# Kernel tuning notes

Measured on AMD Instinct MI355X. Metric: run time of the kernel, lower is better.

## Reference

```python
import jax, jax.numpy as jnp
import numpy as np

N = 8192      # nodes (64 graphs x 128 nodes)
E = 131072    # edges (avg degree 16)
G = 64        # graphs
F_IN = 64     # num_node_features
F_E = 32      # num_edge_features
H0, H1, H2, H3, H4 = 64, 64, 128, 64, 32  # hidden_channels


def setup_inputs() -> dict:
    key = jax.random.key(0)
    ks = jax.random.split(key, 20)
    s = lambda i, shape, sc=0.05: (jax.random.normal(ks[i], shape, dtype=jnp.float32) * sc)
    inp = {
        "x": jax.random.normal(ks[0], (N, F_IN), dtype=jnp.float32),
        "edge_attr": jax.random.normal(ks[1], (E, F_E), dtype=jnp.float32),
        # EdgeMLP: Linear(F_E,128) -> ReLU -> Linear(128,64) -> ReLU -> Linear(64, F_IN*H0)
        "mlp_w1": s(2, (F_E, 128)), "mlp_b1": jnp.zeros((128,), jnp.float32),
        "mlp_w2": s(3, (128, 64)), "mlp_b2": jnp.zeros((64,), jnp.float32),
        "mlp_w3": s(4, (64, F_IN * H0), 0.02), "mlp_b3": jnp.zeros((F_IN * H0,), jnp.float32),
        # NNConv root weight + bias
        "root_w": s(5, (F_IN, H0)), "conv1_b": jnp.zeros((H0,), jnp.float32),
        # GATConv (heads=1, concat=False)
        "gat_w": s(6, (H0, H1)), "att_src": s(7, (H1,)), "att_dst": s(8, (H1,)),
        "gat_b": jnp.zeros((H1,), jnp.float32),
        # dense head
        "fc1_w": s(9, (H1, H2)), "fc1_b": jnp.zeros((H2,), jnp.float32),
        "fc2_w": s(10, (H2, H3)), "fc2_b": jnp.zeros((H3,), jnp.float32),
        "fc3_w": s(11, (H3, H4)), "fc3_b": jnp.zeros((H4,), jnp.float32),
        "edge_index": jax.random.randint(ks[12], (2, E), 0, N, dtype=jnp.int64),
        "batch": jnp.sort(jax.random.randint(ks[13], (N,), 0, G, dtype=jnp.int64)),
    }
    return inp


def reference(x, edge_attr, mlp_w1, mlp_b1, mlp_w2, mlp_b2, mlp_w3, mlp_b3,
              root_w, conv1_b, gat_w, att_src, att_dst, gat_b,
              fc1_w, fc1_b, fc2_w, fc2_b, fc3_w, fc3_b, edge_index, batch):
    src, dst = edge_index[0], edge_index[1]

    # ---- NNConv: edge-MLP -> per-edge weight [E, F_IN, H0], gather-matmul-scatter (aggr='add')
    h = jax.nn.relu(edge_attr @ mlp_w1 + mlp_b1)
    h = jax.nn.relu(h @ mlp_w2 + mlp_b2)
    ew = (h @ mlp_w3 + mlp_b3).reshape(E, F_IN, H0)          # [E, in, out]
    msg = jnp.einsum('ei,eio->eo', x[src], ew)               # per-edge message
    agg = jax.ops.segment_sum(msg, dst, num_segments=N)      # scatter-add to targets
    x1 = jax.nn.relu(agg + x @ root_w + conv1_b)             # root weight + bias, then ReLU

    # ---- GATConv (1 head, concat=False, add_self_loops=True, negative_slope=0.2)
    hg = x1 @ gat_w                                           # [N, H1]
    loop = jnp.arange(N, dtype=src.dtype)
    s2 = jnp.concatenate([src, loop])
    d2 = jnp.concatenate([dst, loop])
    e = jax.nn.leaky_relu(hg[s2] @ att_src + hg[d2] @ att_dst, negative_slope=0.2)
    # segment softmax over incoming edges of each target node
    emax = jax.ops.segment_max(e, d2, num_segments=N)
    ee = jnp.exp(e - emax[d2])
    denom = jax.ops.segment_sum(ee, d2, num_segments=N)
    alpha = ee / denom[d2]
    x2 = jax.ops.segment_sum(alpha[:, None] * hg[s2], d2, num_segments=N) + gat_b
    x2 = jax.nn.relu(x2)

    # ---- global mean pool over graphs, then MLP head
    gsum = jax.ops.segment_sum(x2, batch, num_segments=G)
    cnt = jax.ops.segment_sum(jnp.ones((N,), x2.dtype), batch, num_segments=G)
    g = gsum / jnp.maximum(cnt, 1.0)[:, None]
    g = jax.nn.relu(g @ fc1_w + fc1_b)
    g = jax.nn.relu(g @ fc2_w + fc2_b)
    g = jax.nn.relu(g @ fc3_w + fc3_b)
    return g
```

## Files before the change

kernel.cpp:

```cpp
#include <hip/hip_runtime.h>
#include <math.h>

#define NN 8192
#define NE 131072
#define NG 64
#define FIN 64
#define FE 32

static __device__ __forceinline__ float relu(float v){ return v > 0.f ? v : 0.f; }

__global__ void k_hist(const int* __restrict__ ei, int* scnt, int* dcnt){
  int e = blockIdx.x*256 + threadIdx.x;
  if (e < NE){ atomicAdd(&scnt[ei[e]],1); atomicAdd(&dcnt[ei[NE+e]],1); }
}

__global__ void k_scan(const int* __restrict__ scnt, const int* __restrict__ dcnt,
                       int* soff, int* scur, int* doff, int* dcur){
  const int* cnt = (blockIdx.x==0) ? scnt : dcnt;
  int* off = (blockIdx.x==0) ? soff : doff;
  int* cur = (blockIdx.x==0) ? scur : dcur;
  __shared__ int sums[1024];
  int t = threadIdx.x;
  int v[8]; int s = 0;
  #pragma unroll
  for (int j=0;j<8;++j){ v[j]=cnt[t*8+j]; s+=v[j]; }
  sums[t]=s; __syncthreads();
  for (int d=1; d<1024; d<<=1){
    int val = (t>=d) ? sums[t-d] : 0;
    __syncthreads();
    sums[t] += val;
    __syncthreads();
  }
  int run = sums[t]-s;
  #pragma unroll
  for (int j=0;j<8;++j){ off[t*8+j]=run; cur[t*8+j]=run; run+=v[j]; }
  if (t==1023) off[NN]=run;
}

__global__ void k_scatter(const int* __restrict__ ei, int* scur, int* dcur,
                          int* sperm, int* dperm){
  int e = blockIdx.x*256 + threadIdx.x;
  if (e < NE){
    int s = ei[e], d = ei[NE+e];
    sperm[atomicAdd(&scur[s],1)] = e;
    dperm[atomicAdd(&dcur[d],1)] = e;
  }
}

__global__ __launch_bounds__(256) void k_mlp12(const float* __restrict__ EA,
      const float* __restrict__ W1, const float* __restrict__ B1,
      const float* __restrict__ W2, const float* __restrict__ B2,
      float* __restrict__ H2out){
  __shared__ float W1s[FE*128];
  __shared__ float W2s[128*64];
  __shared__ float B1s[128];
  __shared__ float B2s[64];
  __shared__ float eas[4][4][FE];
  __shared__ float h1s[4][4][128];
  int tid = threadIdx.x;
  int wv = tid >> 6, lane = tid & 63;
  for (int i=tid;i<FE*128;i+=256) W1s[i]=W1[i];
  for (int i=tid;i<128*64;i+=256) W2s[i]=W2[i];
  if (tid<128) B1s[tid]=B1[tid];
  if (tid<64)  B2s[tid]=B2[tid];
  int e0 = (blockIdx.x*4 + wv)*4;
  for (int j=lane;j<4*FE;j+=64) eas[wv][j>>5][j&31] = EA[e0*FE + j];
  __syncthreads();

  float a0[4], a1[4];
  #pragma unroll
  for (int e=0;e<4;++e){ a0[e]=B1s[lane]; a1[e]=B1s[64+lane]; }
  for (int kg=0; kg<8; ++kg){
    float w00=W1s[(kg*4+0)*128+lane],  w01=W1s[(kg*4+0)*128+64+lane];
    float w10=W1s[(kg*4+1)*128+lane],  w11=W1s[(kg*4+1)*128+64+lane];
    float w20=W1s[(kg*4+2)*128+lane],  w21=W1s[(kg*4+2)*128+64+lane];
    float w30=W1s[(kg*4+3)*128+lane],  w31=W1s[(kg*4+3)*128+64+lane];
    #pragma unroll
    for (int e=0;e<4;++e){
      float4 xv = *(const float4*)&eas[wv][e][kg*4];
      a0[e] += xv.x*w00 + xv.y*w10 + xv.z*w20 + xv.w*w30;
      a1[e] += xv.x*w01 + xv.y*w11 + xv.z*w21 + xv.w*w31;
    }
  }
  #pragma unroll
  for (int e=0;e<4;++e){ h1s[wv][e][lane]=relu(a0[e]); h1s[wv][e][64+lane]=relu(a1[e]); }
  __syncthreads();

  float c[4];
  #pragma unroll
  for (int e=0;e<4;++e) c[e]=B2s[lane];
  for (int kg=0; kg<32; ++kg){
    float w0=W2s[(kg*4+0)*64+lane];
    float w1=W2s[(kg*4+1)*64+lane];
    float w2=W2s[(kg*4+2)*64+lane];
    float w3=W2s[(kg*4+3)*64+lane];
    #pragma unroll
    for (int e=0;e<4;++e){
      float4 hv = *(const float4*)&h1s[wv][e][kg*4];
      c[e] += hv.x*w0 + hv.y*w1 + hv.z*w2 + hv.w*w3;
    }
  }
  #pragma unroll
  for (int e=0;e<4;++e) H2out[(size_t)(e0+e)*64+lane] = relu(c[e]);
}

__global__ __launch_bounds__(256) void k_pgen(const float* __restrict__ X,
      const float* __restrict__ W3, float* __restrict__ P){
  __shared__ float xs[16][64];
  int tid = threadIdx.x;
  int kk = tid>>6, o = tid&63;
  int n0 = blockIdx.x*16;
  for (int i=tid;i<16*64;i+=256) xs[i>>6][i&63] = X[(size_t)n0*64+i];
  __syncthreads();
  for (int ko=0; ko<16; ++ko){
    int k = ko*4 + kk;
    const float* wr = W3 + (size_t)k*4096 + o;
    float acc[16];
    #pragma unroll
    for (int n=0;n<16;++n) acc[n]=0.f;
    for (int ig=0; ig<16; ++ig){
      float w0 = wr[(ig*4+0)*64];
      float w1 = wr[(ig*4+1)*64];
      float w2 = wr[(ig*4+2)*64];
      float w3v= wr[(ig*4+3)*64];
      #pragma unroll
      for (int n=0;n<16;++n){
        float4 xv = *(const float4*)&xs[n][ig*4];
        acc[n] += xv.x*w0 + xv.y*w1 + xv.z*w2 + xv.w*w3v;
      }
    }
    float* pr = P + (size_t)n0*4096 + k*64 + o;
    #pragma unroll
    for (int n=0;n<16;++n) pr[(size_t)n*4096] = acc[n];
  }
}

__global__ __launch_bounds__(256) void k_root(const float* __restrict__ X,
      const float* __restrict__ RW, const float* __restrict__ CB,
      const float* __restrict__ B3, float* __restrict__ AGG, float* __restrict__ XB){
  int tid=threadIdx.x, wv=tid>>6, lane=tid&63;
  int n = blockIdx.x*4 + wv;
  __shared__ float xr[4][64];
  xr[wv][lane] = X[(size_t)n*64+lane];
  __syncthreads();
  float aA = CB[lane], aB = 0.f;
  for (int ig=0; ig<16; ++ig){
    float4 xv = *(const float4*)&xr[wv][ig*4];
    int i0 = ig*4;
    aA += xv.x*RW[(i0+0)*64+lane] + xv.y*RW[(i0+1)*64+lane]
        + xv.z*RW[(i0+2)*64+lane] + xv.w*RW[(i0+3)*64+lane];
    aB += xv.x*B3[(i0+0)*64+lane] + xv.y*B3[(i0+1)*64+lane]
        + xv.z*B3[(i0+2)*64+lane] + xv.w*B3[(i0+3)*64+lane];
  }
  AGG[(size_t)n*64+lane]=aA; XB[(size_t)n*64+lane]=aB;
}

__global__ __launch_bounds__(64) void k_msg(const float* __restrict__ P,
      const float* __restrict__ H2v, const float* __restrict__ XB,
      const int* __restrict__ ei, const int* __restrict__ soff,
      const int* __restrict__ sperm, float* __restrict__ AGG){
  __shared__ float Pl[4096];
  __shared__ float h2r[64];
  int lane = threadIdx.x;
  int n = blockIdx.x;
  const float4* ps = (const float4*)(P + (size_t)n*4096);
  float4* pl = (float4*)Pl;
  for (int i=lane;i<1024;i+=64) pl[i]=ps[i];
  float xbv = XB[(size_t)n*64+lane];
  int beg = soff[n], end = soff[n+1];
  __syncthreads();
  for (int idx=beg; idx<end; ++idx){
    int e = sperm[idx];
    h2r[lane] = H2v[(size_t)e*64+lane];
    __syncthreads();
    float acc = xbv;
    for (int kg=0;kg<16;++kg){
      float4 hv = *(const float4*)&h2r[kg*4];
      acc += hv.x*Pl[(kg*4+0)*64+lane] + hv.y*Pl[(kg*4+1)*64+lane]
           + hv.z*Pl[(kg*4+2)*64+lane] + hv.w*Pl[(kg*4+3)*64+lane];
    }
    int d = ei[NE+e];
    atomicAdd(&AGG[(size_t)d*64+lane], acc);
    __syncthreads();
  }
}

__global__ __launch_bounds__(256) void k_hg(const float* __restrict__ AGG,
      const float* __restrict__ GW, const float* __restrict__ ASRC,
      const float* __restrict__ ADST, float* __restrict__ HG,
      float* __restrict__ AS, float* __restrict__ AD){
  int tid=threadIdx.x, wv=tid>>6, lane=tid&63;
  int n = blockIdx.x*4+wv;
  __shared__ float xr[4][64];
  xr[wv][lane] = relu(AGG[(size_t)n*64+lane]);
  __syncthreads();
  float acc=0.f;
  for (int ig=0; ig<16; ++ig){
    float4 xv = *(const float4*)&xr[wv][ig*4];
    int i0=ig*4;
    acc += xv.x*GW[(i0+0)*64+lane] + xv.y*GW[(i0+1)*64+lane]
         + xv.z*GW[(i0+2)*64+lane] + xv.w*GW[(i0+3)*64+lane];
  }
  HG[(size_t)n*64+lane]=acc;
  float t1 = acc*ASRC[lane], t2 = acc*ADST[lane];
  #pragma unroll
  for (int d=32; d>=1; d>>=1){ t1 += __shfl_xor(t1,d); t2 += __shfl_xor(t2,d); }
  if (lane==0){ AS[n]=t1; AD[n]=t2; }
}

__global__ __launch_bounds__(64) void k_gat(const float* __restrict__ HG,
      const float* __restrict__ AS, const float* __restrict__ AD,
      const float* __restrict__ GB, const int* __restrict__ ei,
      const int* __restrict__ doff, const int* __restrict__ dperm,
      float* __restrict__ X2){
  int lane = threadIdx.x;
  int n = blockIdx.x;
  int beg = doff[n], end = doff[n+1], deg = end-beg;
  float adn = AD[n];
  float selfsc = AS[n] + adn; selfsc = selfsc>0.f ? selfsc : 0.2f*selfsc;
  float lmax = -3.4e38f;
  for (int j=lane; j<deg; j+=64){
    int e = dperm[beg+j];
    float sc = AS[ei[e]] + adn; sc = sc>0.f ? sc : 0.2f*sc;
    lmax = fmaxf(lmax, sc);
  }
  #pragma unroll
  for (int d=32; d>=1; d>>=1) lmax = fmaxf(lmax, __shfl_xor(lmax,d));
  float mx = fmaxf(lmax, selfsc);
  float lsum = 0.f;
  for (int j=lane; j<deg; j+=64){
    int e = dperm[beg+j];
    float sc = AS[ei[e]] + adn; sc = sc>0.f ? sc : 0.2f*sc;
    lsum += expf(sc-mx);
  }
  #pragma unroll
  for (int d=32; d>=1; d>>=1) lsum += __shfl_xor(lsum,d);
  float wself = expf(selfsc-mx);
  float denom = lsum + wself;
  float acc = wself * HG[(size_t)n*64+lane];
  for (int idx=beg; idx<end; ++idx){
    int e = dperm[idx];
    int s = ei[e];
    float sc = AS[s] + adn; sc = sc>0.f ? sc : 0.2f*sc;
    float wgt = expf(sc-mx);
    acc += wgt * HG[(size_t)s*64+lane];
  }
  X2[(size_t)n*64+lane] = relu(acc/denom + GB[lane]);
}

__global__ __launch_bounds__(64) void k_head(const float* __restrict__ X2,
      const int* __restrict__ batch,
      const float* __restrict__ F1W, const float* __restrict__ F1B,
      const float* __restrict__ F2W, const float* __restrict__ F2B,
      const float* __restrict__ F3W, const float* __restrict__ F3B,
      float* __restrict__ OUT){
  int lane = threadIdx.x;
  int g = blockIdx.x;
  int lo=0, hi=NN;
  while (lo<hi){ int m=(lo+hi)>>1; if (batch[m] < g) lo=m+1; else hi=m; }
  int start = lo;
  lo=0; hi=NN;
  while (lo<hi){ int m=(lo+hi)>>1; if (batch[m] < g+1) lo=m+1; else hi=m; }
  int stop = lo;
  float s = 0.f;
  for (int r=start; r<stop; ++r) s += X2[(size_t)r*64+lane];
  float cnt = (float)(stop-start);
  float mean = s / fmaxf(cnt, 1.f);
  __shared__ float ms[64];
  __shared__ float g1[128];
  __shared__ float g2[64];
  ms[lane]=mean;
  __syncthreads();
  float a0=F1B[lane], a1=F1B[64+lane];
  for (int ig=0; ig<16; ++ig){
    float4 mv = *(const float4*)&ms[ig*4];
    int i0=ig*4;
    a0 += mv.x*F1W[(i0+0)*128+lane] + mv.y*F1W[(i0+1)*128+lane]
        + mv.z*F1W[(i0+2)*128+lane] + mv.w*F1W[(i0+3)*128+lane];
    a1 += mv.x*F1W[(i0+0)*128+64+lane] + mv.y*F1W[(i0+1)*128+64+lane]
        + mv.z*F1W[(i0+2)*128+64+lane] + mv.w*F1W[(i0+3)*128+64+lane];
  }
  g1[lane]=relu(a0); g1[64+lane]=relu(a1);
  __syncthreads();
  float b = F2B[lane];
  for (int kg=0; kg<32; ++kg){
    float4 gv = *(const float4*)&g1[kg*4];
    int k0=kg*4;
    b += gv.x*F2W[(k0+0)*64+lane] + gv.y*F2W[(k0+1)*64+lane]
       + gv.z*F2W[(k0+2)*64+lane] + gv.w*F2W[(k0+3)*64+lane];
  }
  g2[lane]=relu(b);
  __syncthreads();
  if (lane < 32){
    float cc = F3B[lane];
    for (int kg=0; kg<16; ++kg){
      float4 gv = *(const float4*)&g2[kg*4];
      int k0=kg*4;
      cc += gv.x*F3W[(k0+0)*32+lane] + gv.y*F3W[(k0+1)*32+lane]
          + gv.z*F3W[(k0+2)*32+lane] + gv.w*F3W[(k0+3)*32+lane];
    }
    OUT[g*32+lane] = relu(cc);
  }
}

extern "C" void kernel_launch(void* const* d_in, const int* in_sizes, int n_in,
                              void* d_out, int out_size, void* d_ws, size_t ws_size,
                              hipStream_t stream){
  const float* X   = (const float*)d_in[0];
  const float* EA  = (const float*)d_in[1];
  const float* W1  = (const float*)d_in[2];
  const float* B1  = (const float*)d_in[3];
  const float* W2  = (const float*)d_in[4];
  const float* B2  = (const float*)d_in[5];
  const float* W3  = (const float*)d_in[6];
  const float* B3  = (const float*)d_in[7];
  const float* RW  = (const float*)d_in[8];
  const float* CB  = (const float*)d_in[9];
  const float* GW  = (const float*)d_in[10];
  const float* ASRC= (const float*)d_in[11];
  const float* ADST= (const float*)d_in[12];
  const float* GB  = (const float*)d_in[13];
  const float* F1W = (const float*)d_in[14];
  const float* F1B = (const float*)d_in[15];
  const float* F2W = (const float*)d_in[16];
  const float* F2B = (const float*)d_in[17];
  const float* F3W = (const float*)d_in[18];
  const float* F3B = (const float*)d_in[19];
  const int*   EI  = (const int*)d_in[20];
  const int*   BATCH = (const int*)d_in[21];
  float* OUT = (float*)d_out;
  (void)in_sizes; (void)n_in; (void)out_size; (void)ws_size;

  char* w = (char*)d_ws;
  size_t off = 0;
  auto alloc = [&](size_t bytes)->char*{
    char* p = w + off; off = (off + bytes + 255) & ~(size_t)255; return p;
  };
  float* P    = (float*)alloc((size_t)NN*4096*4);
  float* H2v  = (float*)alloc((size_t)NE*64*4);
  float* XB   = (float*)alloc((size_t)NN*64*4);
  float* AGG  = (float*)alloc((size_t)NN*64*4);
  float* HGv  = (float*)alloc((size_t)NN*64*4);
  float* X2   = (float*)alloc((size_t)NN*64*4);
  float* AS   = (float*)alloc((size_t)NN*4);
  float* AD   = (float*)alloc((size_t)NN*4);
  int* scnt = (int*)alloc((size_t)NN*4);
  int* dcnt = (int*)alloc((size_t)NN*4);
  int* soff = (int*)alloc((size_t)(NN+1)*4);
  int* doff = (int*)alloc((size_t)(NN+1)*4);
  int* scur = (int*)alloc((size_t)NN*4);
  int* dcur = (int*)alloc((size_t)NN*4);
  int* sperm= (int*)alloc((size_t)NE*4);
  int* dperm= (int*)alloc((size_t)NE*4);

  hipMemsetAsync(scnt, 0, NN*4, stream);
  hipMemsetAsync(dcnt, 0, NN*4, stream);
  k_hist<<<NE/256,256,0,stream>>>(EI, scnt, dcnt);
  k_scan<<<2,1024,0,stream>>>(scnt,dcnt,soff,scur,doff,dcur);
  k_scatter<<<NE/256,256,0,stream>>>(EI,scur,dcur,sperm,dperm);
  k_mlp12<<<NE/16,256,0,stream>>>(EA,W1,B1,W2,B2,H2v);
  k_pgen<<<NN/16,256,0,stream>>>(X,W3,P);
  k_root<<<NN/4,256,0,stream>>>(X,RW,CB,B3,AGG,XB);
  k_msg<<<NN,64,0,stream>>>(P,H2v,XB,EI,soff,sperm,AGG);
  k_hg<<<NN/4,256,0,stream>>>(AGG,GW,ASRC,ADST,HGv,AS,AD);
  k_gat<<<NN,64,0,stream>>>(HGv,AS,AD,GB,EI,doff,dperm,X2);
  k_head<<<NG,64,0,stream>>>(X2,BATCH,F1W,F1B,F2W,F2B,F3W,F3B,OUT);
}
```

Before: 553.0 us.

## Replace LDS staging with register-resident weights and readlane broadcasts across kernels

Rewrites the dense matmul-style kernels (edge MLP, P generation, root, message, GAT projection, head) to keep weights and per-node P rows in registers and broadcast activations with the readlane builtin instead of shared memory and __syncthreads. The edge MLP now loads weights once per block and loops over 8 tiles of edges, and pgen uses 512-thread blocks over 8 nodes. The message kernel skips nodes with no outgoing edges and drops per-edge barriers. This trades LDS traffic and barriers for heavy register pressure and scalar readlane instructions, which may limit occupancy or cause spills.

```diff
diff --git a/kernel.cpp b/kernel.cpp
--- a/kernel.cpp
+++ b/kernel.cpp
@@ -8,6 +8,10 @@
 #define FE 32
 
 static __device__ __forceinline__ float relu(float v){ return v > 0.f ? v : 0.f; }
+
+static __device__ __forceinline__ float rdlane(float v, int l){
+  return __int_as_float(__builtin_amdgcn_readlane(__float_as_int(v), l));
+}
 
 __global__ void k_hist(const int* __restrict__ ei, int* scnt, int* dcnt){
   int e = blockIdx.x*256 + threadIdx.x;
@@ -47,92 +51,89 @@
   }
 }
 
-__global__ __launch_bounds__(256) void k_mlp12(const float* __restrict__ EA,
+__global__ __launch_bounds__(256,2) void k_mlp12(const float* __restrict__ EA,
       const float* __restrict__ W1, const float* __restrict__ B1,
       const float* __restrict__ W2, const float* __restrict__ B2,
       float* __restrict__ H2out){
-  __shared__ float W1s[FE*128];
-  __shared__ float W2s[128*64];
-  __shared__ float B1s[128];
-  __shared__ float B2s[64];
-  __shared__ float eas[4][4][FE];
-  __shared__ float h1s[4][4][128];
-  int tid = threadIdx.x;
-  int wv = tid >> 6, lane = tid & 63;
-  for (int i=tid;i<FE*128;i+=256) W1s[i]=W1[i];
-  for (int i=tid;i<128*64;i+=256) W2s[i]=W2[i];
-  if (tid<128) B1s[tid]=B1[tid];
-  if (tid<64)  B2s[tid]=B2[tid];
-  int e0 = (blockIdx.x*4 + wv)*4;
-  for (int j=lane;j<4*FE;j+=64) eas[wv][j>>5][j&31] = EA[e0*FE + j];
-  __syncthreads();
-
-  float a0[4], a1[4];
-  #pragma unroll
-  for (int e=0;e<4;++e){ a0[e]=B1s[lane]; a1[e]=B1s[64+lane]; }
-  for (int kg=0; kg<8; ++kg){
-    float w00=W1s[(kg*4+0)*128+lane],  w01=W1s[(kg*4+0)*128+64+lane];
-    float w10=W1s[(kg*4+1)*128+lane],  w11=W1s[(kg*4+1)*128+64+lane];
-    float w20=W1s[(kg*4+2)*128+lane],  w21=W1s[(kg*4+2)*128+64+lane];
-    float w30=W1s[(kg*4+3)*128+lane],  w31=W1s[(kg*4+3)*128+64+lane];
-    #pragma unroll
-    for (int e=0;e<4;++e){
-      float4 xv = *(const float4*)&eas[wv][e][kg*4];
-      a0[e] += xv.x*w00 + xv.y*w10 + xv.z*w20 + xv.w*w30;
-      a1[e] += xv.x*w01 + xv.y*w11 + xv.z*w21 + xv.w*w31;
-    }
-  }
-  #pragma unroll
-  for (int e=0;e<4;++e){ h1s[wv][e][lane]=relu(a0[e]); h1s[wv][e][64+lane]=relu(a1[e]); }
-  __syncthreads();
-
-  float c[4];
-  #pragma unroll
-  for (int e=0;e<4;++e) c[e]=B2s[lane];
-  for (int kg=0; kg<32; ++kg){
-    float w0=W2s[(kg*4+0)*64+lane];
-    float w1=W2s[(kg*4+1)*64+lane];
-    float w2=W2s[(kg*4+2)*64+lane];
-    float w3=W2s[(kg*4+3)*64+lane];
-    #pragma unroll
-    for (int e=0;e<4;++e){
-      float4 hv = *(const float4*)&h1s[wv][e][kg*4];
-      c[e] += hv.x*w0 + hv.y*w1 + hv.z*w2 + hv.w*w3;
-    }
-  }
-  #pragma unroll
-  for (int e=0;e<4;++e) H2out[(size_t)(e0+e)*64+lane] = relu(c[e]);
-}
-
-__global__ __launch_bounds__(256) void k_pgen(const float* __restrict__ X,
-      const float* __restrict__ W3, float* __restrict__ P){
-  __shared__ float xs[16][64];
-  int tid = threadIdx.x;
-  int kk = tid>>6, o = tid&63;
-  int n0 = blockIdx.x*16;
-  for (int i=tid;i<16*64;i+=256) xs[i>>6][i&63] = X[(size_t)n0*64+i];
-  __syncthreads();
-  for (int ko=0; ko<16; ++ko){
-    int k = ko*4 + kk;
-    const float* wr = W3 + (size_t)k*4096 + o;
-    float acc[16];
-    #pragma unroll
-    for (int n=0;n<16;++n) acc[n]=0.f;
-    for (int ig=0; ig<16; ++ig){
-      float w0 = wr[(ig*4+0)*64];
-      float w1 = wr[(ig*4+1)*64];
-      float w2 = wr[(ig*4+2)*64];
-      float w3v= wr[(ig*4+3)*64];
+  int tid=threadIdx.x, wv=tid>>6, lane=tid&63;
+  float w1a[32], w1b[32], w2r[128];
+  #pragma unroll
+  for (int i=0;i<32;++i){ w1a[i]=W1[i*128+lane]; w1b[i]=W1[i*128+64+lane]; }
+  #pragma unroll
+  for (int k=0;k<128;++k) w2r[k]=W2[k*64+lane];
+  float b1a=B1[lane], b1b=B1[64+lane], b2v=B2[lane];
+
+  #pragma unroll 1
+  for (int t=0;t<8;++t){
+    int e0 = blockIdx.x*128 + t*16 + wv*4;
+    float r0 = EA[(size_t)e0*32 + lane];
+    float r1 = EA[(size_t)e0*32 + 64 + lane];
+    float a0[4], a1[4];
+    #pragma unroll
+    for (int e=0;e<4;++e){ a0[e]=b1a; a1[e]=b1b; }
+    #pragma unroll
+    for (int i=0;i<32;++i){
       #pragma unroll
-      for (int n=0;n<16;++n){
-        float4 xv = *(const float4*)&xs[n][ig*4];
-        acc[n] += xv.x*w0 + xv.y*w1 + xv.z*w2 + xv.w*w3v;
+      for (int e=0;e<4;++e){
+        const int f = e*32+i;
+        float sx = rdlane((f<64)?r0:r1, f&63);
+        a0[e] += sx*w1a[i];
+        a1[e] += sx*w1b[i];
       }
     }
-    float* pr = P + (size_t)n0*4096 + k*64 + o;
-    #pragma unroll
-    for (int n=0;n<16;++n) pr[(size_t)n*4096] = acc[n];
-  }
+    #pragma unroll
+    for (int e=0;e<4;++e){ a0[e]=relu(a0[e]); a1[e]=relu(a1[e]); }
+    float c[4];
+    #pragma unroll
+    for (int e=0;e<4;++e) c[e]=b2v;
+    #pragma unroll
+    for (int k=0;k<64;++k){
+      #pragma unroll
+      for (int e=0;e<4;++e) c[e] += rdlane(a0[e],k)*w2r[k];
+    }
+    #pragma unroll
+    for (int k=0;k<64;++k){
+      #pragma unroll
+      for (int e=0;e<4;++e) c[e] += rdlane(a1[e],k)*w2r[64+k];
+    }
+    #pragma unroll
+    for (int e=0;e<4;++e) H2out[(size_t)(e0+e)*64+lane] = relu(c[e]);
+  }
+}
+
+__global__ __launch_bounds__(512,4) void k_pgen(const float* __restrict__ X,
+      const float* __restrict__ W3, float* __restrict__ P){
+  int tid = threadIdx.x;
+  int kk = tid>>6, lane = tid&63;
+  int n0 = blockIdx.x*8;
+  float xv[8];
+  #pragma unroll
+  for (int n=0;n<8;++n) xv[n] = X[(size_t)(n0+n)*64 + lane];
+  float acc[8][8];
+  #pragma unroll
+  for (int n=0;n<8;++n)
+    #pragma unroll
+    for (int j=0;j<8;++j) acc[n][j]=0.f;
+  const float* wb = W3 + (size_t)(kk*8)*4096 + lane;
+  #pragma unroll 4
+  for (int i=0;i<64;++i){
+    float w[8];
+    #pragma unroll
+    for (int j=0;j<8;++j) w[j] = wb[(size_t)j*4096 + i*64];
+    float sx[8];
+    #pragma unroll
+    for (int n=0;n<8;++n) sx[n] = rdlane(xv[n], i);
+    #pragma unroll
+    for (int n=0;n<8;++n)
+      #pragma unroll
+      for (int j=0;j<8;++j) acc[n][j] += sx[n]*w[j];
+  }
+  float* pb = P + (size_t)n0*4096 + (size_t)kk*8*64 + lane;
+  #pragma unroll
+  for (int n=0;n<8;++n)
+    #pragma unroll
+    for (int j=0;j<8;++j)
+      pb[(size_t)n*4096 + j*64] = acc[n][j];
 }
 
 __global__ __launch_bounds__(256) void k_root(const float* __restrict__ X,
@@ -140,17 +141,13 @@
       const float* __restrict__ B3, float* __restrict__ AGG, float* __restrict__ XB){
   int tid=threadIdx.x, wv=tid>>6, lane=tid&63;
   int n = blockIdx.x*4 + wv;
-  __shared__ float xr[4][64];
-  xr[wv][lane] = X[(size_t)n*64+lane];
-  __syncthreads();
+  float xr = X[(size_t)n*64+lane];
   float aA = CB[lane], aB = 0.f;
-  for (int ig=0; ig<16; ++ig){
-    float4 xv = *(const float4*)&xr[wv][ig*4];
-    int i0 = ig*4;
-    aA += xv.x*RW[(i0+0)*64+lane] + xv.y*RW[(i0+1)*64+lane]
-        + xv.z*RW[(i0+2)*64+lane] + xv.w*RW[(i0+3)*64+lane];
-    aB += xv.x*B3[(i0+0)*64+lane] + xv.y*B3[(i0+1)*64+lane]
-        + xv.z*B3[(i0+2)*64+lane] + xv.w*B3[(i0+3)*64+lane];
+  #pragma unroll
+  for (int i=0;i<64;++i){
+    float sx = rdlane(xr, i);
+    aA += sx*RW[i*64+lane];
+    aB += sx*B3[i*64+lane];
   }
   AGG[(size_t)n*64+lane]=aA; XB[(size_t)n*64+lane]=aB;
 }
@@ -159,29 +156,24 @@
       const float* __restrict__ H2v, const float* __restrict__ XB,
       const int* __restrict__ ei, const int* __restrict__ soff,
       const int* __restrict__ sperm, float* __restrict__ AGG){
-  __shared__ float Pl[4096];
-  __shared__ float h2r[64];
   int lane = threadIdx.x;
   int n = blockIdx.x;
-  const float4* ps = (const float4*)(P + (size_t)n*4096);
-  float4* pl = (float4*)Pl;
-  for (int i=lane;i<1024;i+=64) pl[i]=ps[i];
+  int beg = soff[n], end = soff[n+1];
+  if (beg==end) return;
+  float pr[64];
+  const float* pb = P + (size_t)n*4096 + lane;
+  #pragma unroll
+  for (int k=0;k<64;++k) pr[k] = pb[k*64];
   float xbv = XB[(size_t)n*64+lane];
-  int beg = soff[n], end = soff[n+1];
-  __syncthreads();
+  #pragma unroll 1
   for (int idx=beg; idx<end; ++idx){
     int e = sperm[idx];
-    h2r[lane] = H2v[(size_t)e*64+lane];
-    __syncthreads();
+    float h = H2v[(size_t)e*64+lane];
+    int d = ei[NE+e];
     float acc = xbv;
-    for (int kg=0;kg<16;++kg){
-      float4 hv = *(const float4*)&h2r[kg*4];
-      acc += hv.x*Pl[(kg*4+0)*64+lane] + hv.y*Pl[(kg*4+1)*64+lane]
-           + hv.z*Pl[(kg*4+2)*64+lane] + hv.w*Pl[(kg*4+3)*64+lane];
-    }
-    int d = ei[NE+e];
+    #pragma unroll
+    for (int k=0;k<64;++k) acc += rdlane(h,k)*pr[k];
     atomicAdd(&AGG[(size_t)d*64+lane], acc);
-    __syncthreads();
   }
 }
 
@@ -191,15 +183,11 @@
       float* __restrict__ AS, float* __restrict__ AD){
   int tid=threadIdx.x, wv=tid>>6, lane=tid&63;
   int n = blockIdx.x*4+wv;
-  __shared__ float xr[4][64];
-  xr[wv][lane] = relu(AGG[(size_t)n*64+lane]);
-  __syncthreads();
+  float xr = relu(AGG[(size_t)n*64+lane]);
   float acc=0.f;
-  for (int ig=0; ig<16; ++ig){
-    float4 xv = *(const float4*)&xr[wv][ig*4];
-    int i0=ig*4;
-    acc += xv.x*GW[(i0+0)*64+lane] + xv.y*GW[(i0+1)*64+lane]
-         + xv.z*GW[(i0+2)*64+lane] + xv.w*GW[(i0+3)*64+lane];
+  #pragma unroll
+  for (int i=0;i<64;++i){
+    acc += rdlane(xr,i)*GW[i*64+lane];
   }
   HG[(size_t)n*64+lane]=acc;
   float t1 = acc*ASRC[lane], t2 = acc*ADST[lane];
@@ -266,41 +254,30 @@
   for (int r=start; r<stop; ++r) s += X2[(size_t)r*64+lane];
   float cnt = (float)(stop-start);
   float mean = s / fmaxf(cnt, 1.f);
-  __shared__ float ms[64];
-  __shared__ float g1[128];
-  __shared__ float g2[64];
-  ms[lane]=mean;
-  __syncthreads();
   float a0=F1B[lane], a1=F1B[64+lane];
-  for (int ig=0; ig<16; ++ig){
-    float4 mv = *(const float4*)&ms[ig*4];
-    int i0=ig*4;
-    a0 += mv.x*F1W[(i0+0)*128+lane] + mv.y*F1W[(i0+1)*128+lane]
-        + mv.z*F1W[(i0+2)*128+lane] + mv.w*F1W[(i0+3)*128+lane];
-    a1 += mv.x*F1W[(i0+0)*128+64+lane] + mv.y*F1W[(i0+1)*128+64+lane]
-        + mv.z*F1W[(i0+2)*128+64+lane] + mv.w*F1W[(i0+3)*128+64+lane];
-  }
-  g1[lane]=relu(a0); g1[64+lane]=relu(a1);
-  __syncthreads();
+  #pragma unroll
+  for (int i=0;i<64;++i){
+    float mv = rdlane(mean, i);
+    a0 += mv*F1W[i*128+lane];
+    a1 += mv*F1W[i*128+64+lane];
+  }
+  float g1a = relu(a0), g1b = relu(a1);
   float b = F2B[lane];
-  for (int kg=0; kg<32; ++kg){
-    float4 gv = *(const float4*)&g1[kg*4];
-    int k0=kg*4;
-    b += gv.x*F2W[(k0+0)*64+lane] + gv.y*F2W[(k0+1)*64+lane]
-       + gv.z*F2W[(k0+2)*64+lane] + gv.w*F2W[(k0+3)*64+lane];
-  }
-  g2[lane]=relu(b);
-  __syncthreads();
-  if (lane < 32){
-    float cc = F3B[lane];
-    for (int kg=0; kg<16; ++kg){
-      float4 gv = *(const float4*)&g2[kg*4];
-      int k0=kg*4;
-      cc += gv.x*F3W[(k0+0)*32+lane] + gv.y*F3W[(k0+1)*32+lane]
-          + gv.z*F3W[(k0+2)*32+lane] + gv.w*F3W[(k0+3)*32+lane];
-    }
-    OUT[g*32+lane] = relu(cc);
-  }
+  #pragma unroll
+  for (int k=0;k<64;++k){
+    b += rdlane(g1a,k)*F2W[k*64+lane];
+  }
+  #pragma unroll
+  for (int k=0;k<64;++k){
+    b += rdlane(g1b,k)*F2W[(64+k)*64+lane];
+  }
+  float g2v = relu(b);
+  float cc = (lane<32) ? F3B[lane] : 0.f;
+  #pragma unroll
+  for (int k=0;k<64;++k){
+    cc += rdlane(g2v,k)*F3W[k*32+(lane&31)];
+  }
+  if (lane < 32) OUT[g*32+lane] = relu(cc);
 }
 
 extern "C" void kernel_launch(void* const* d_in, const int* in_sizes, int n_in,
@@ -358,8 +335,8 @@
   k_hist<<<NE/256,256,0,stream>>>(EI, scnt, dcnt);
   k_scan<<<2,1024,0,stream>>>(scnt,dcnt,soff,scur,doff,dcur);
   k_scatter<<<NE/256,256,0,stream>>>(EI,scur,dcur,sperm,dperm);
-  k_mlp12<<<NE/16,256,0,stream>>>(EA,W1,B1,W2,B2,H2v);
-  k_pgen<<<NN/16,256,0,stream>>>(X,W3,P);
+  k_mlp12<<<NE/128,256,0,stream>>>(EA,W1,B1,W2,B2,H2v);
+  k_pgen<<<NN/8,512,0,stream>>>(X,W3,P);
   k_root<<<NN/4,256,0,stream>>>(X,RW,CB,B3,AGG,XB);
   k_msg<<<NN,64,0,stream>>>(P,H2v,XB,EI,soff,sperm,AGG);
   k_hg<<<NN/4,256,0,stream>>>(AGG,GW,ASRC,ADST,HGv,AS,AD);
```

After: 1.010 ms. +82.6%, slower.
